# Kernel optimization log

Measured on AMD Instinct MI355X. Metric: run time of the kernel, lower is better.

Reference implementation:

```python
import jax, jax.numpy as jnp
import numpy as np

N, IN_F, HID, HEADS, OUT = 50000, 128, 32, 4, 40
E = 800000
LN_EPS = 1e-5


def setup_inputs() -> dict:
    key = jax.random.key(0)
    ks = jax.random.split(key, 16)
    d1 = HEADS * HID  # 128
    s_in = 1.0 / np.sqrt(IN_F)
    s_d1 = 1.0 / np.sqrt(d1)
    return {
        "x": jax.random.normal(ks[0], (N, IN_F), jnp.float32),
        "edge_index": jax.random.randint(ks[1], (2, E), 0, N, jnp.int64),
        # layer 1 (GATv2, heads=4, concat=True)
        "Wl1": jax.random.normal(ks[2], (IN_F, d1), jnp.float32) * s_in,
        "bl1": jnp.zeros((d1,), jnp.float32),
        "Wr1": jax.random.normal(ks[3], (IN_F, d1), jnp.float32) * s_in,
        "br1": jnp.zeros((d1,), jnp.float32),
        "att1": jax.random.normal(ks[4], (HEADS, HID), jnp.float32) * s_d1,
        "b1": jnp.zeros((d1,), jnp.float32),
        # LayerNorm over hidden_channels*heads
        "g1": jnp.ones((d1,), jnp.float32),
        "be1": jnp.zeros((d1,), jnp.float32),
        # layer 2 (GATv2, heads=1, concat=False)
        "Wl2": jax.random.normal(ks[5], (d1, OUT), jnp.float32) * s_d1,
        "bl2": jnp.zeros((OUT,), jnp.float32),
        "Wr2": jax.random.normal(ks[6], (d1, OUT), jnp.float32) * s_d1,
        "br2": jnp.zeros((OUT,), jnp.float32),
        "att2": jax.random.normal(ks[7], (1, OUT), jnp.float32) / np.sqrt(OUT),
        "b2": jnp.zeros((OUT,), jnp.float32),
    }


def gatv2(x, src, tgt, Wl, bl, Wr, br, att, bias, heads, C, concat):
    n = x.shape[0]
    xl = (x @ Wl + bl).reshape(n, heads, C)  # source transform
    xr = (x @ Wr + br).reshape(n, heads, C)  # target transform
    h = xl[src] + xr[tgt]                    # [E,H,C]
    e = jnp.sum(jax.nn.leaky_relu(h, 0.2) * att, axis=-1)  # [E,H]
    # segment softmax over edges sharing the same target node
    m = jax.ops.segment_max(e, tgt, num_segments=n)        # [N,H]
    m = jnp.where(jnp.isfinite(m), m, 0.0)
    p = jnp.exp(e - m[tgt])
    s = jax.ops.segment_sum(p, tgt, num_segments=n)
    alpha = p / (s[tgt] + 1e-16)                           # [E,H]
    out = jax.ops.segment_sum(alpha[..., None] * xl[src], tgt, num_segments=n)  # [N,H,C]
    out = out.reshape(n, heads * C) if concat else out.mean(axis=1)
    return out + bias


def layer_norm(x, g, b):
    mu = x.mean(-1, keepdims=True)
    var = x.var(-1, keepdims=True)
    return (x - mu) * jax.lax.rsqrt(var + LN_EPS) * g + b


def reference(x, edge_index, Wl1, bl1, Wr1, br1, att1, b1, g1, be1,
              Wl2, bl2, Wr2, br2, att2, b2):
    src, tgt = edge_index[0], edge_index[1]
    h = gatv2(x, src, tgt, Wl1, bl1, Wr1, br1, att1, b1, HEADS, HID, True)
    h = jax.nn.elu(layer_norm(h, g1, be1))
    # dropout is identity in eval mode
    return gatv2(h, src, tgt, Wl2, bl2, Wr2, br2, att2, b2, 1, OUT, False)
```

## Files before the change

### kernel.cpp

```cpp
#include <hip/hip_runtime.h>
#include <hip/hip_bf16.h>
#include <math.h>

#define NN 50000
#define EE 800000
#define NB_SCAN 49

typedef __attribute__((ext_vector_type(8))) short bf16x8;
typedef __attribute__((ext_vector_type(4))) float f32x4;
typedef __attribute__((ext_vector_type(8))) unsigned short ushortx8;

#define OFF_XBF   ((size_t)0)
#define OFF_XL2B  ((size_t)0)
#define OFF_XR2   ((size_t)4000000)
#define OFF_XL1B  ((size_t)12800000)
#define OFF_H1B   ((size_t)12800000)
#define OFF_XR1   ((size_t)25600000)
#define OFF_H1PRE ((size_t)51200000)
#define OFF_S1    ((size_t)76800000)
#define OFF_BP1   ((size_t)77600000)
#define OFF_BP2   ((size_t)77665536)
#define OFF_BB1   ((size_t)77686016)
#define OFF_BB2   ((size_t)77687040)
#define OFF_DEG   ((size_t)77687552)
#define OFF_OFFS  ((size_t)77887552)
#define OFF_BSUM  ((size_t)78087808)
#define OFF_CSR   ((size_t)78088064)
#define OFF_RANK  ((size_t)81288064)

__device__ __forceinline__ unsigned short f2bf(float f) {
    union { float f; unsigned u; } v;
    v.f = f;
    unsigned r = v.u + 0x7fffu + ((v.u >> 16) & 1u);
    return (unsigned short)(r >> 16);
}
__device__ __forceinline__ float bfl(unsigned u) {
    union { unsigned u; float f; } v;
    v.u = u << 16;
    return v.f;
}
__device__ __forceinline__ float bfh(unsigned u) {
    union { unsigned u; float f; } v;
    v.u = u & 0xffff0000u;
    return v.f;
}
__device__ __forceinline__ float lrelu02(float h) { return fmaxf(h, 0.2f * h); }

__global__ void prep_kernel(
    const float* __restrict__ x, unsigned short* __restrict__ XBF,
    const int* __restrict__ tgts, int* __restrict__ DEG, int* __restrict__ RANK,
    const float* __restrict__ Wl1, const float* __restrict__ bl1,
    const float* __restrict__ Wr1, const float* __restrict__ br1,
    const float* __restrict__ Wl2, const float* __restrict__ bl2,
    const float* __restrict__ Wr2, const float* __restrict__ br2,
    unsigned short* __restrict__ BP1, float* __restrict__ BB1,
    unsigned short* __restrict__ BP2, float* __restrict__ BB2) {
    int i = blockIdx.x * blockDim.x + threadIdx.x;
    if (i < NN * 128 / 8) {
        const float4* p = (const float4*)x + (size_t)i * 2;
        float4 v0 = p[0], v1 = p[1];
        ushortx8 o;
        o[0] = f2bf(v0.x); o[1] = f2bf(v0.y); o[2] = f2bf(v0.z); o[3] = f2bf(v0.w);
        o[4] = f2bf(v1.x); o[5] = f2bf(v1.y); o[6] = f2bf(v1.z); o[7] = f2bf(v1.w);
        *((ushortx8*)XBF + i) = o;
    }
    if (i < EE) RANK[i] = atomicAdd(&DEG[tgts[i]], 1);
    if (i < 32768) {
        int j = i & 7, l = (i >> 3) & 63, nt = (i >> 9) & 15, kt = i >> 13;
        int k = kt * 32 + ((l >> 4) << 3) + j;
        int n = nt * 16 + (l & 15);
        float v = (n < 128) ? Wl1[k * 128 + n] : Wr1[k * 128 + (n - 128)];
        BP1[i] = f2bf(v);
    }
    if (i < 10240) {
        int j = i & 7, l = (i >> 3) & 63;
        int rest = i >> 9;
        int nt = rest % 5, kt = rest / 5;
        int k = kt * 32 + ((l >> 4) << 3) + j;
        int n = nt * 16 + (l & 15);
        float v = (n < 40) ? Wl2[k * 40 + n] : Wr2[k * 40 + (n - 40)];
        BP2[i] = f2bf(v);
    }
    if (i < 256) BB1[i] = (i < 128) ? bl1[i] : br1[i - 128];
    if (i < 80) BB2[i] = (i < 40) ? bl2[i] : br2[i - 40];
}

__global__ __launch_bounds__(1024) void scan_bsum_kernel(
    const int* __restrict__ deg, int* __restrict__ bsum, int n) {
    __shared__ int ws[16];
    int lane = threadIdx.x & 63, w = threadIdx.x >> 6;
    int i = blockIdx.x * 1024 + threadIdx.x;
    int v = (i < n) ? deg[i] : 0;
#pragma unroll
    for (int d = 32; d >= 1; d >>= 1) v += __shfl_xor(v, d, 64);
    if (lane == 0) ws[w] = v;
    __syncthreads();
    if (threadIdx.x < 16) {
        int xv = ws[threadIdx.x];
#pragma unroll
        for (int d = 8; d >= 1; d >>= 1) xv += __shfl_xor(xv, d, 16);
        if (threadIdx.x == 0) bsum[blockIdx.x] = xv;
    }
}

__global__ __launch_bounds__(1024) void scan_final_kernel(
    const int* __restrict__ deg, const int* __restrict__ bsum,
    int* __restrict__ off, int n) {
    __shared__ int wsum[16];
    __shared__ int carrySh;
    int lane = threadIdx.x & 63, w = threadIdx.x >> 6;
    if (threadIdx.x < 64) {
        int v = ((int)threadIdx.x < (int)blockIdx.x) ? bsum[threadIdx.x] : 0;
#pragma unroll
        for (int d = 32; d >= 1; d >>= 1) v += __shfl_xor(v, d, 64);
        if (threadIdx.x == 0) carrySh = v;
    }
    int i = blockIdx.x * 1024 + threadIdx.x;
    int v = (i < n) ? deg[i] : 0;
    int incl = v;
#pragma unroll
    for (int d = 1; d < 64; d <<= 1) {
        int t = __shfl_up(incl, d, 64);
        if (lane >= d) incl += t;
    }
    if (lane == 63) wsum[w] = incl;
    __syncthreads();
    if (threadIdx.x < 16) {
        int xv = wsum[threadIdx.x];
#pragma unroll
        for (int d = 1; d < 16; d <<= 1) {
            int t = __shfl_up(xv, d, 16);
            if ((int)threadIdx.x >= d) xv += t;
        }
        wsum[threadIdx.x] = xv;
    }
    __syncthreads();
    int add = (w > 0) ? wsum[w - 1] : 0;
    int carry = carrySh;
    if (i < n) off[i + 1] = carry + incl + add;
    if (i == 0) off[0] = 0;
}

__global__ void scatter_kernel(const int* __restrict__ srcs, const int* __restrict__ tgts,
                               const int* __restrict__ off, const int* __restrict__ rank,
                               int* __restrict__ csr, int e_) {
    int e = blockIdx.x * blockDim.x + threadIdx.x;
    if (e < e_) {
        int pos = off[tgts[e]] + rank[e];
        csr[pos] = srcs[e];
    }
}

__global__ __launch_bounds__(256) void gemm_mfma_kernel(
    const unsigned short* __restrict__ Abf, const unsigned short* __restrict__ BP,
    const float* __restrict__ bias, unsigned short* __restrict__ Cbf,
    float* __restrict__ Cf, int M, int NT, int NSPLIT) {
    int wave = (blockIdx.x * blockDim.x + threadIdx.x) >> 6;
    int lane = threadIdx.x & 63;
    int r0 = wave * 16;
    if (r0 >= M) return;
    int koff = (lane >> 4) << 3;
    const unsigned short* ap = &Abf[(size_t)(r0 + (lane & 15)) * 128 + koff];
    bf16x8 a0 = *(const bf16x8*)(ap);
    bf16x8 a1 = *(const bf16x8*)(ap + 32);
    bf16x8 a2 = *(const bf16x8*)(ap + 64);
    bf16x8 a3 = *(const bf16x8*)(ap + 96);
    int NR = (NT << 4) - NSPLIT;
    int col = lane & 15;
    int rb = r0 + ((lane >> 4) << 2);
    size_t ktStride = (size_t)NT * 512;
    for (int nt = 0; nt < NT; ++nt) {
        const unsigned short* bp = &BP[((size_t)nt * 64 + lane) * 8];
        f32x4 acc = {0.f, 0.f, 0.f, 0.f};
        acc = __builtin_amdgcn_mfma_f32_16x16x32_bf16(a0, *(const bf16x8*)(bp), acc, 0, 0, 0);
        acc = __builtin_amdgcn_mfma_f32_16x16x32_bf16(a1, *(const bf16x8*)(bp + ktStride), acc, 0, 0, 0);
        acc = __builtin_amdgcn_mfma_f32_16x16x32_bf16(a2, *(const bf16x8*)(bp + 2 * ktStride), acc, 0, 0, 0);
        acc = __builtin_amdgcn_mfma_f32_16x16x32_bf16(a3, *(const bf16x8*)(bp + 3 * ktStride), acc, 0, 0, 0);
        int c = (nt << 4) + col;
        float bb = bias[c];
        if (c < NSPLIT) {
#pragma unroll
            for (int j = 0; j < 4; ++j) Cbf[(size_t)(rb + j) * NSPLIT + c] = f2bf(acc[j] + bb);
        } else {
#pragma unroll
            for (int j = 0; j < 4; ++j) Cf[(size_t)(rb + j) * NR + (c - NSPLIT)] = acc[j] + bb;
        }
    }
}

__global__ __launch_bounds__(256) void gat_head1_kernel(
    const unsigned short* __restrict__ XL1B, const float* __restrict__ XR1,
    const int* __restrict__ off, const int* __restrict__ csr,
    const float* __restrict__ att, float* __restrict__ H1pre,
    float* __restrict__ S1, int cb) {
    int wid = threadIdx.x >> 6;
    int lane = threadIdx.x & 63;
    int node = blockIdx.x * 4 + wid;
    if (node >= NN) return;
    int grp = lane >> 4;
    int sub = lane & 15;
    int coff = cb * 32 + sub * 2;
    float2 xr = *(const float2*)&XR1[(size_t)node * 128 + coff];
    float2 at = *(const float2*)&att[coff];
    const unsigned short* base = XL1B + coff;
    float a0 = 0.f, a1 = 0.f, sl = 0.f;
    int jb = off[node], je = off[node + 1];
    int deg = je - jb;

    auto proc = [&](int srcv, int eo) {
        unsigned u = *(const unsigned*)(base + (size_t)srcv * 128);
        float x0 = bfl(u), x1 = bfh(u);
        float t = lrelu02(x0 + xr.x) * at.x;
        t = fmaf(lrelu02(x1 + xr.y), at.y, t);
        t += __shfl_xor(t, 1, 64);
        t += __shfl_xor(t, 2, 64);
        t += __shfl_xor(t, 4, 64);
        t += __shfl_xor(t, 8, 64);
        t = (eo < deg) ? t : -1e30f;
        float p = __expf(t);
        a0 = fmaf(p, x0, a0);
        a1 = fmaf(p, x1, a1);
        sl += p;
    };

    for (int ch = 0; ch < deg; ch += 16) {
        int sidx = csr[min(jb + ch + sub, je - 1)];
        int s0 = __shfl(sidx, grp, 16);
        int s1 = __shfl(sidx, 4 + grp, 16);
        int s2 = __shfl(sidx, 8 + grp, 16);
        int s3 = __shfl(sidx, 12 + grp, 16);
        proc(s0, ch + grp);
        proc(s1, ch + 4 + grp);
        proc(s2, ch + 8 + grp);
        proc(s3, ch + 12 + grp);
    }
#pragma unroll
    for (int d = 16; d <= 32; d <<= 1) {
        a0 += __shfl_xor(a0, d, 64);
        a1 += __shfl_xor(a1, d, 64);
        sl += __shfl_xor(sl, d, 64);
    }
    if (grp == 0) {
        float2 v;
        v.x = a0;
        v.y = a1;
        *(float2*)&H1pre[(size_t)node * 128 + coff] = v;
        if (sub == 0) S1[node * 4 + cb] = sl;
    }
}

__global__ __launch_bounds__(256) void ln1_kernel(
    const float* __restrict__ H1pre, const float* __restrict__ S1,
    const float* __restrict__ b1, const float* __restrict__ g1,
    const float* __restrict__ be1, unsigned short* __restrict__ H1B) {
    int wid = threadIdx.x >> 6;
    int lane = threadIdx.x & 63;
    int node = blockIdx.x * 4 + wid;
    if (node >= NN) return;
    int c = lane * 2;
    float2 v = *(const float2*)&H1pre[(size_t)node * 128 + c];
    float sl = S1[node * 4 + (lane >> 4)];
    float inv = 1.f / (sl + 1e-16f);
    float o0 = v.x * inv + b1[c];
    float o1 = v.y * inv + b1[c + 1];
    float sum = o0 + o1, sq = o0 * o0 + o1 * o1;
#pragma unroll
    for (int d = 32; d >= 1; d >>= 1) {
        sum += __shfl_xor(sum, d, 64);
        sq += __shfl_xor(sq, d, 64);
    }
    float mu = sum * (1.f / 128.f);
    float var = sq * (1.f / 128.f) - mu * mu;
    float rs = rsqrtf(var + 1e-5f);
    float y0 = (o0 - mu) * rs * g1[c] + be1[c];
    float y1 = (o1 - mu) * rs * g1[c + 1] + be1[c + 1];
    y0 = y0 > 0.f ? y0 : expm1f(y0);
    y1 = y1 > 0.f ? y1 : expm1f(y1);
    unsigned o = (unsigned)f2bf(y0) | ((unsigned)f2bf(y1) << 16);
    ((unsigned*)H1B)[(size_t)node * 64 + lane] = o;
}

__global__ __launch_bounds__(256) void gat_edge2_kernel(
    const unsigned short* __restrict__ XL2B, const float* __restrict__ XR2,
    const int* __restrict__ off, const int* __restrict__ csr,
    const float* __restrict__ att2, const float* __restrict__ b2,
    float* __restrict__ Y) {
    int wid = threadIdx.x >> 6;
    int lane = threadIdx.x & 63;
    int node = blockIdx.x * 4 + wid;
    if (node >= NN) return;
    int grp = lane >> 4;
    int sub = lane & 15;
    bool chact = sub < 10;
    int cld = chact ? sub * 4 : 0;
    float4 xr = make_float4(0.f, 0.f, 0.f, 0.f);
    float4 at = make_float4(0.f, 0.f, 0.f, 0.f);
    if (chact) {
        xr = *(const float4*)&XR2[(size_t)node * 40 + cld];
        at = *(const float4*)&att2[cld];
    }
    float a0 = 0.f, a1 = 0.f, a2 = 0.f, a3 = 0.f, sl = 0.f;
    int jb = off[node], je = off[node + 1];
    int deg = je - jb;

    auto proc = [&](int srcv, int eo) {
        uint2 u = *(const uint2*)(XL2B + (size_t)srcv * 40 + cld);
        float x0 = bfl(u.x), x1 = bfh(u.x), x2 = bfl(u.y), x3 = bfh(u.y);
        float t = lrelu02(x0 + xr.x) * at.x;
        t = fmaf(lrelu02(x1 + xr.y), at.y, t);
        t = fmaf(lrelu02(x2 + xr.z), at.z, t);
        t = fmaf(lrelu02(x3 + xr.w), at.w, t);
        t += __shfl_xor(t, 1, 64);
        t += __shfl_xor(t, 2, 64);
        t += __shfl_xor(t, 4, 64);
        t += __shfl_xor(t, 8, 64);
        t = (eo < deg) ? t : -1e30f;
        float p = __expf(t);
        a0 = fmaf(p, x0, a0);
        a1 = fmaf(p, x1, a1);
        a2 = fmaf(p, x2, a2);
        a3 = fmaf(p, x3, a3);
        sl += p;
    };

    for (int ch = 0; ch < deg; ch += 16) {
        int sidx = csr[min(jb + ch + sub, je - 1)];
        int s0 = __shfl(sidx, grp, 16);
        int s1 = __shfl(sidx, 4 + grp, 16);
        int s2 = __shfl(sidx, 8 + grp, 16);
        int s3 = __shfl(sidx, 12 + grp, 16);
        proc(s0, ch + grp);
        proc(s1, ch + 4 + grp);
        proc(s2, ch + 8 + grp);
        proc(s3, ch + 12 + grp);
    }
#pragma unroll
    for (int d = 16; d <= 32; d <<= 1) {
        a0 += __shfl_xor(a0, d, 64);
        a1 += __shfl_xor(a1, d, 64);
        a2 += __shfl_xor(a2, d, 64);
        a3 += __shfl_xor(a3, d, 64);
        sl += __shfl_xor(sl, d, 64);
    }
    if (grp == 0 && chact) {
        float inv = 1.f / (sl + 1e-16f);
        float4 y;
        y.x = a0 * inv + b2[cld];
        y.y = a1 * inv + b2[cld + 1];
        y.z = a2 * inv + b2[cld + 2];
        y.w = a3 * inv + b2[cld + 3];
        *(float4*)&Y[(size_t)node * 40 + cld] = y;
    }
}

extern "C" void kernel_launch(void* const* d_in, const int* in_sizes, int n_in,
                              void* d_out, int out_size, void* d_ws, size_t ws_size,
                              hipStream_t stream) {
    const float* x = (const float*)d_in[0];
    const int* ei = (const int*)d_in[1];
    const float* Wl1 = (const float*)d_in[2];
    const float* bl1 = (const float*)d_in[3];
    const float* Wr1 = (const float*)d_in[4];
    const float* br1 = (const float*)d_in[5];
    const float* att1 = (const float*)d_in[6];
    const float* b1 = (const float*)d_in[7];
    const float* g1 = (const float*)d_in[8];
    const float* be1 = (const float*)d_in[9];
    const float* Wl2 = (const float*)d_in[10];
    const float* bl2 = (const float*)d_in[11];
    const float* Wr2 = (const float*)d_in[12];
    const float* br2 = (const float*)d_in[13];
    const float* att2 = (const float*)d_in[14];
    const float* b2 = (const float*)d_in[15];

    const int* srcs = ei;
    const int* tgts = ei + EE;

    char* ws = (char*)d_ws;
    unsigned short* XBF = (unsigned short*)(ws + OFF_XBF);
    unsigned short* XL2B = (unsigned short*)(ws + OFF_XL2B);
    float* XR2 = (float*)(ws + OFF_XR2);
    unsigned short* XL1B = (unsigned short*)(ws + OFF_XL1B);
    unsigned short* H1B = (unsigned short*)(ws + OFF_H1B);
    float* XR1 = (float*)(ws + OFF_XR1);
    float* H1pre = (float*)(ws + OFF_H1PRE);
    float* S1 = (float*)(ws + OFF_S1);
    unsigned short* BP1 = (unsigned short*)(ws + OFF_BP1);
    unsigned short* BP2 = (unsigned short*)(ws + OFF_BP2);
    float* BB1 = (float*)(ws + OFF_BB1);
    float* BB2 = (float*)(ws + OFF_BB2);
    int* DEG = (int*)(ws + OFF_DEG);
    int* OFFS = (int*)(ws + OFF_OFFS);
    int* BSUM = (int*)(ws + OFF_BSUM);
    int* CSR = (int*)(ws + OFF_CSR);
    int* RANK = (int*)(ws + OFF_RANK);

    float* Y = (float*)d_out;

    hipMemsetAsync(DEG, 0, NN * sizeof(int), stream);
    prep_kernel<<<(NN * 128 / 8 + 255) / 256, 256, 0, stream>>>(
        x, XBF, tgts, DEG, RANK, Wl1, bl1, Wr1, br1, Wl2, bl2, Wr2, br2,
        BP1, BB1, BP2, BB2);

    scan_bsum_kernel<<<NB_SCAN, 1024, 0, stream>>>(DEG, BSUM, NN);
    scan_final_kernel<<<NB_SCAN, 1024, 0, stream>>>(DEG, BSUM, OFFS, NN);
    scatter_kernel<<<(EE + 255) / 256, 256, 0, stream>>>(srcs, tgts, OFFS, RANK, CSR, EE);

    gemm_mfma_kernel<<<(3125 + 3) / 4, 256, 0, stream>>>(XBF, BP1, BB1, XL1B, XR1, NN, 16, 128);

    for (int cb = 0; cb < 4; ++cb)
        gat_head1_kernel<<<12500, 256, 0, stream>>>(XL1B, XR1, OFFS, CSR, att1, H1pre, S1, cb);

    ln1_kernel<<<12500, 256, 0, stream>>>(H1pre, S1, b1, g1, be1, H1B);

    gemm_mfma_kernel<<<(3125 + 3) / 4, 256, 0, stream>>>(H1B, BP2, BB2, XL2B, XR2, NN, 5, 40);

    gat_edge2_kernel<<<(NN + 3) / 4, 256, 0, stream>>>(XL2B, XR2, OFFS, CSR, att2, b2, Y);
}
```

Baseline: 235.2 us.

## Replace global-atomic CSR build with block-local LDS counting sort

```diff
diff --git a/kernel.cpp b/kernel.cpp
--- a/kernel.cpp
+++ b/kernel.cpp
@@ -5,6 +5,8 @@
 #define NN 50000
 #define EE 800000
 #define NB_SCAN 49
+#define NBLK_CS 64
+#define EPB (EE / NBLK_CS)
 
 typedef __attribute__((ext_vector_type(8))) short bf16x8;
 typedef __attribute__((ext_vector_type(4))) float f32x4;
@@ -16,6 +18,8 @@
 #define OFF_XL1B  ((size_t)12800000)
 #define OFF_H1B   ((size_t)12800000)
 #define OFF_XR1   ((size_t)25600000)
+#define OFF_HB    ((size_t)51200000)
+#define OFF_BOFF  ((size_t)54400000)
 #define OFF_H1PRE ((size_t)51200000)
 #define OFF_S1    ((size_t)76800000)
 #define OFF_BP1   ((size_t)77600000)
@@ -26,7 +30,6 @@
 #define OFF_OFFS  ((size_t)77887552)
 #define OFF_BSUM  ((size_t)78087808)
 #define OFF_CSR   ((size_t)78088064)
-#define OFF_RANK  ((size_t)81288064)
 
 __device__ __forceinline__ unsigned short f2bf(float f) {
     union { float f; unsigned u; } v;
@@ -48,7 +51,6 @@
 
 __global__ void prep_kernel(
     const float* __restrict__ x, unsigned short* __restrict__ XBF,
-    const int* __restrict__ tgts, int* __restrict__ DEG, int* __restrict__ RANK,
     const float* __restrict__ Wl1, const float* __restrict__ bl1,
     const float* __restrict__ Wr1, const float* __restrict__ br1,
     const float* __restrict__ Wl2, const float* __restrict__ bl2,
@@ -64,7 +66,6 @@
         o[4] = f2bf(v1.x); o[5] = f2bf(v1.y); o[6] = f2bf(v1.z); o[7] = f2bf(v1.w);
         *((ushortx8*)XBF + i) = o;
     }
-    if (i < EE) RANK[i] = atomicAdd(&DEG[tgts[i]], 1);
     if (i < 32768) {
         int j = i & 7, l = (i >> 3) & 63, nt = (i >> 9) & 15, kt = i >> 13;
         int k = kt * 32 + ((l >> 4) << 3) + j;
@@ -85,6 +86,54 @@
     if (i < 80) BB2[i] = (i < 40) ? bl2[i] : br2[i - 40];
 }
 
+__global__ __launch_bounds__(1024) void cs_hist_kernel(
+    const int* __restrict__ tgts, unsigned char* __restrict__ HB) {
+    __shared__ unsigned int cnt[NN / 4];
+    int b = blockIdx.x;
+    for (int i = threadIdx.x; i < NN / 4; i += 1024) cnt[i] = 0;
+    __syncthreads();
+    int e0 = b * EPB;
+    for (int i = threadIdx.x; i < EPB; i += 1024) {
+        int t = tgts[e0 + i];
+        atomicAdd(&cnt[t >> 2], 1u << ((t & 3) * 8));
+    }
+    __syncthreads();
+    unsigned int* out = (unsigned int*)(HB + (size_t)b * NN);
+    for (int i = threadIdx.x; i < NN / 4; i += 1024) out[i] = cnt[i];
+}
+
+__global__ void cs_boff_kernel(const unsigned char* __restrict__ HB,
+                               int* __restrict__ BOFF, int* __restrict__ DEG) {
+    int t = blockIdx.x * 256 + threadIdx.x;
+    if (t >= NN) return;
+    int run = 0;
+#pragma unroll
+    for (int b = 0; b < NBLK_CS; ++b) {
+        BOFF[(size_t)b * NN + t] = run;
+        run += HB[(size_t)b * NN + t];
+    }
+    DEG[t] = run;
+}
+
+__global__ __launch_bounds__(1024) void cs_scatter_kernel(
+    const int* __restrict__ srcs, const int* __restrict__ tgts,
+    const int* __restrict__ off, const int* __restrict__ boff,
+    int* __restrict__ csr) {
+    __shared__ unsigned int cnt[NN / 4];
+    int b = blockIdx.x;
+    for (int i = threadIdx.x; i < NN / 4; i += 1024) cnt[i] = 0;
+    __syncthreads();
+    int e0 = b * EPB;
+    const int* bo = boff + (size_t)b * NN;
+    for (int i = threadIdx.x; i < EPB; i += 1024) {
+        int t = tgts[e0 + i];
+        int sh = (t & 3) * 8;
+        unsigned old = atomicAdd(&cnt[t >> 2], 1u << sh);
+        int r = (old >> sh) & 0xFF;
+        csr[off[t] + bo[t] + r] = srcs[e0 + i];
+    }
+}
+
 __global__ __launch_bounds__(1024) void scan_bsum_kernel(
     const int* __restrict__ deg, int* __restrict__ bsum, int n) {
     __shared__ int ws[16];
@@ -139,16 +188,6 @@
     int carry = carrySh;
     if (i < n) off[i + 1] = carry + incl + add;
     if (i == 0) off[0] = 0;
-}
-
-__global__ void scatter_kernel(const int* __restrict__ srcs, const int* __restrict__ tgts,
-                               const int* __restrict__ off, const int* __restrict__ rank,
-                               int* __restrict__ csr, int e_) {
-    int e = blockIdx.x * blockDim.x + threadIdx.x;
-    if (e < e_) {
-        int pos = off[tgts[e]] + rank[e];
-        csr[pos] = srcs[e];
-    }
 }
 
 __global__ __launch_bounds__(256) void gemm_mfma_kernel(
@@ -383,6 +422,8 @@
     unsigned short* XL1B = (unsigned short*)(ws + OFF_XL1B);
     unsigned short* H1B = (unsigned short*)(ws + OFF_H1B);
     float* XR1 = (float*)(ws + OFF_XR1);
+    unsigned char* HB = (unsigned char*)(ws + OFF_HB);
+    int* BOFF = (int*)(ws + OFF_BOFF);
     float* H1pre = (float*)(ws + OFF_H1PRE);
     float* S1 = (float*)(ws + OFF_S1);
     unsigned short* BP1 = (unsigned short*)(ws + OFF_BP1);
@@ -393,18 +434,17 @@
     int* OFFS = (int*)(ws + OFF_OFFS);
     int* BSUM = (int*)(ws + OFF_BSUM);
     int* CSR = (int*)(ws + OFF_CSR);
-    int* RANK = (int*)(ws + OFF_RANK);
 
     float* Y = (float*)d_out;
 
-    hipMemsetAsync(DEG, 0, NN * sizeof(int), stream);
     prep_kernel<<<(NN * 128 / 8 + 255) / 256, 256, 0, stream>>>(
-        x, XBF, tgts, DEG, RANK, Wl1, bl1, Wr1, br1, Wl2, bl2, Wr2, br2,
-        BP1, BB1, BP2, BB2);
-
+        x, XBF, Wl1, bl1, Wr1, br1, Wl2, bl2, Wr2, br2, BP1, BB1, BP2, BB2);
+
+    cs_hist_kernel<<<NBLK_CS, 1024, 0, stream>>>(tgts, HB);
+    cs_boff_kernel<<<(NN + 255) / 256, 256, 0, stream>>>(HB, BOFF, DEG);
     scan_bsum_kernel<<<NB_SCAN, 1024, 0, stream>>>(DEG, BSUM, NN);
     scan_final_kernel<<<NB_SCAN, 1024, 0, stream>>>(DEG, BSUM, OFFS, NN);
-    scatter_kernel<<<(EE + 255) / 256, 256, 0, stream>>>(srcs, tgts, OFFS, RANK, CSR, EE);
+    cs_scatter_kernel<<<NBLK_CS, 1024, 0, stream>>>(srcs, tgts, OFFS, BOFF, CSR);
 
     gemm_mfma_kernel<<<(3125 + 3) / 4, 256, 0, stream>>>(XBF, BP1, BB1, XL1B, XR1, NN, 16, 128);
 
```

Measured after the change: 241.0 us. 1.02x slower.
